# Kernel optimization log

Hardware: AMD Instinct MI355X
Metric: run time of the kernel (lower is better)

The kernel has to match this reference:

```python
import jax, jax.numpy as jnp
import numpy as np

N, E = 25000, 400000
F, D, H, C, L = 64, 128, 4, 128, 3  # in_feat, hidden, heads, per-head dim, layers
SCALE = 1.0 / np.sqrt(C)

_PNAMES = [f"{nm}{l}" for l in range(L) for nm in ("Wq", "bq", "Wk", "bk", "Wv", "bv", "Ws", "bs")]


def setup_inputs() -> dict:
    key = jax.random.key(0)
    ks = jax.random.split(key, 64)
    inp = {
        "x": jax.random.normal(ks[0], (N, F), jnp.float32),
        "edge_index": jax.random.randint(ks[1], (2, E), 0, N, jnp.int32),
    }
    i = 2
    for l in range(L):
        fin = F if l == 0 else D
        s = 1.0 / np.sqrt(fin)
        shapes = {"Wq": (fin, H * C), "bq": (H * C,), "Wk": (fin, H * C), "bk": (H * C,),
                  "Wv": (fin, H * C), "bv": (H * C,), "Ws": (fin, D), "bs": (D,)}
        for nm, shp in shapes.items():
            scale = s if nm.startswith("W") else 0.01
            inp[f"{nm}{l}"] = jax.random.normal(ks[i], shp, jnp.float32) * scale
            i += 1
    inp["Wfc"] = jax.random.normal(ks[i], (D, 1), jnp.float32) * (1.0 / np.sqrt(D))
    inp["bfc"] = jnp.zeros((1,), jnp.float32)
    return inp


def _conv(x, src, dst, Wq, bq, Wk, bk, Wv, bv, Ws, bs):
    """PyG TransformerConv, heads=H, concat=False (head-mean), root_weight=True."""
    n = x.shape[0]
    q = (x @ Wq + bq).reshape(n, H, C)
    k = (x @ Wk + bk).reshape(n, H, C)
    v = (x @ Wv + bv).reshape(n, H, C)
    # per-edge attention logits: query at dst, key at src  -> [E, H]
    alpha = jnp.einsum("ehc,ehc->eh", q[dst], k[src]) * SCALE
    # scatter-softmax over incoming edges of each destination node
    m = jax.ops.segment_max(alpha, dst, num_segments=n)        # [N, H]
    e = jnp.exp(alpha - m[dst])                                 # [E, H]
    denom = jax.ops.segment_sum(e, dst, num_segments=n)        # [N, H]
    a = e / (denom[dst] + 1e-16)                                # [E, H]
    out = jax.ops.segment_sum(a[:, :, None] * v[src], dst, num_segments=n)  # [N, H, C]
    return out.mean(axis=1) + x @ Ws + bs                       # concat=False -> mean heads; + skip


def reference(x, edge_index,
              Wq0, bq0, Wk0, bk0, Wv0, bv0, Ws0, bs0,
              Wq1, bq1, Wk1, bk1, Wv1, bv1, Ws1, bs1,
              Wq2, bq2, Wk2, bk2, Wv2, bv2, Ws2, bs2,
              Wfc, bfc):
    src, dst = edge_index[0], edge_index[1]
    h = jax.nn.relu(_conv(x, src, dst, Wq0, bq0, Wk0, bk0, Wv0, bv0, Ws0, bs0))
    h = jax.nn.relu(_conv(h, src, dst, Wq1, bq1, Wk1, bk1, Wv1, bv1, Ws1, bs1))
    h = jax.nn.relu(_conv(h, src, dst, Wq2, bq2, Wk2, bk2, Wv2, bv2, Ws2, bs2))
    g = h.mean(axis=0, keepdims=True)                           # [1, D]
    return jax.nn.sigmoid(g @ Wfc + bfc)                        # [1, 1]
```

## Files before the change

### kernel.cpp

```cpp
#include <hip/hip_runtime.h>
#include <hip/hip_bf16.h>
#include <math.h>

#define NNODES 25000
#define NEDGES 400000
#define FIN0 64
#define DHID 128
#define NHEAD 4
#define CDIM 128
#define HC (NHEAD * CDIM)
#define NOUT 1664
#define SCALE 0.088388347648318447f

typedef __attribute__((ext_vector_type(8))) short short8;
typedef __attribute__((ext_vector_type(4))) float floatx4;
typedef __attribute__((ext_vector_type(2))) float fx2;

__device__ __forceinline__ short f2bf(float v) {
    unsigned u = __float_as_uint(v);
    u = (u + 0x7fffu + ((u >> 16) & 1u)) >> 16;
    return (short)u;
}
__device__ __forceinline__ float bf2f(short s) {
    return __uint_as_float(((unsigned)(unsigned short)s) << 16);
}


__global__ void cvt_x_kernel(const float* __restrict__ x, short* __restrict__ xb, int total) {
    int i = blockIdx.x * blockDim.x + threadIdx.x;
    if (i < total) xb[i] = f2bf(x[i]);
}

__global__ __launch_bounds__(256) void cvt_w_kernel(
    const float* __restrict__ Wq, const float* __restrict__ Wk,
    const float* __restrict__ Wv, const float* __restrict__ Ws,
    const float* __restrict__ bq, const float* __restrict__ bk,
    const float* __restrict__ bv, const float* __restrict__ bs,
    short* __restrict__ WT, float* __restrict__ bc, int fin)
{
    __shared__ float tile[32][33];
    int c0 = blockIdx.x * 32;
    int k0 = blockIdx.y * 32;
    int tx = threadIdx.x & 31, ty = threadIdx.x >> 5;

    const float* W; int ldw, cb;
    if (c0 < 512)       { W = Wq; ldw = 512; cb = c0; }
    else if (c0 < 1024) { W = Wk; ldw = 512; cb = c0 - 512; }
    else if (c0 < 1536) { W = Wv; ldw = 512; cb = c0 - 1024; }
    else                { W = Ws; ldw = 128; cb = c0 - 1536; }

#pragma unroll
    for (int i = 0; i < 4; ++i) {
        int k = k0 + ty + i * 8;
        tile[ty + i * 8][tx] = W[(size_t)k * ldw + cb + tx];
    }
    __syncthreads();
#pragma unroll
    for (int i = 0; i < 4; ++i) {
        int c = c0 + ty + i * 8;
        WT[(size_t)c * fin + k0 + tx] = f2bf(tile[tx][ty + i * 8]);
    }

    if (blockIdx.y == 0 && ty == 0) {
        int c = c0 + tx;
        float b;
        if (c < 512)       b = bq[c];
        else if (c < 1024) b = bk[c - 512];
        else if (c < 1536) b = bv[c - 1024];
        else               b = bs[c - 1536];
        bc[c] = b;
    }
}


__global__ void count_kernel(const int* __restrict__ dst, int* __restrict__ deg, int e) {
    int i = blockIdx.x * blockDim.x + threadIdx.x;
    if (i < e) atomicAdd(&deg[dst[i]], 1);
}

__global__ void scan_kernel(const int* __restrict__ deg, int* __restrict__ offs,
                            int* __restrict__ cnt, int n, int total) {
    __shared__ int sums[256];
    int t = threadIdx.x;
    int chunk = (n + 255) / 256;
    int b = t * chunk;
    int e = min(b + chunk, n);
    int s = 0;
    for (int i = b; i < e; ++i) s += deg[i];
    sums[t] = s;
    __syncthreads();
    for (int o = 1; o < 256; o <<= 1) {
        int v = (t >= o) ? sums[t - o] : 0;
        __syncthreads();
        sums[t] += v;
        __syncthreads();
    }
    int run = sums[t] - s;
    for (int i = b; i < e; ++i) {
        offs[i] = run;
        run += deg[i];
        cnt[i] = 0;
    }
    if (t == 0) offs[n] = total;
}

__global__ void scatter_kernel(const int* __restrict__ src, const int* __restrict__ dst,
                               const int* __restrict__ offs, int* __restrict__ cnt,
                               int* __restrict__ csr, int e) {
    int i = blockIdx.x * blockDim.x + threadIdx.x;
    if (i < e) {
        int d = dst[i];
        int pos = offs[d] + atomicAdd(&cnt[d], 1);
        csr[pos] = src[i];
    }
}

template<int FIN>
__global__ __launch_bounds__(256) void gemm_qkvs_mfma(
    const short* __restrict__ Xb, int n,
    const short* __restrict__ WT, const float* __restrict__ bc,
    short* __restrict__ Qb, unsigned char* __restrict__ KV,
    short* __restrict__ Sb)
{
    constexpr int PITCH = FIN + 8;
    constexpr int CPR = FIN / 8;
    constexpr int NK = FIN / 32;
    __shared__ short Xs[64][PITCH];

    int t = threadIdx.x;
    int row0 = blockIdx.x * 64;
    int l = t & 63, w = t >> 6;
    int wcol = blockIdx.y * 256 + w * 64;
    bool active = (wcol < NOUT);
    int lr = l & 15, lk = (l >> 4) * 8;
    int cl = lr, rb = (l >> 4) * 4;

    short8 bfr[NK][4];
    if (active) {
#pragma unroll
        for (int ks = 0; ks < NK; ++ks)
#pragma unroll
            for (int ni = 0; ni < 4; ++ni)
                bfr[ks][ni] = *(const short8*)&WT[(size_t)(wcol + ni * 16 + lr) * FIN + ks * 32 + lk];
    }

    for (int i = t; i < 64 * CPR; i += 256) {
        int r = i / CPR, c = (i % CPR) * 8;
        int gr = row0 + r;
        uint4 v = make_uint4(0u, 0u, 0u, 0u);
        if (gr < n) v = *(const uint4*)&Xb[(size_t)gr * FIN + c];
        *(uint4*)&Xs[r][c] = v;
    }
    __syncthreads();
    if (!active) return;

    float bias[4];
#pragma unroll
    for (int ni = 0; ni < 4; ++ni) bias[ni] = bc[wcol + ni * 16 + cl];

    floatx4 acc[4][4] = {};
#pragma unroll
    for (int ks = 0; ks < NK; ++ks) {
        short8 a[4];
#pragma unroll
        for (int mi = 0; mi < 4; ++mi)
            a[mi] = *(const short8*)&Xs[mi * 16 + lr][ks * 32 + lk];
#pragma unroll
        for (int mi = 0; mi < 4; ++mi)
#pragma unroll
            for (int ni = 0; ni < 4; ++ni)
                acc[mi][ni] = __builtin_amdgcn_mfma_f32_16x16x32_bf16(
                    a[mi], bfr[ks][ni], acc[mi][ni], 0, 0, 0);
    }

    int kind = (wcol < 512) ? 0 : (wcol < 1024) ? 1 : (wcol < 1536) ? 2 : 3;
#pragma unroll
    for (int mi = 0; mi < 4; ++mi) {
#pragma unroll
        for (int ni = 0; ni < 4; ++ni) {
            int gc = wcol + ni * 16 + cl;
#pragma unroll
            for (int r = 0; r < 4; ++r) {
                int gr = row0 + mi * 16 + rb + r;
                if (gr >= n) continue;
                float v = acc[mi][ni][r] + bias[ni];
                if (kind == 0) {
                    Qb[(size_t)gr * 512 + gc] = f2bf(v);
                } else if (kind == 1) {
                    int c = gc - 512;
                    unsigned enc = (unsigned)__builtin_amdgcn_cvt_pk_fp8_f32(v, v, 0, false);
                    KV[(size_t)gr * 1024 + (c >> 3) * 16 + (c & 7)] = (unsigned char)enc;
                } else if (kind == 2) {
                    int c = gc - 1024;
                    unsigned enc = (unsigned)__builtin_amdgcn_cvt_pk_fp8_f32(v, v, 0, false);
                    KV[(size_t)gr * 1024 + (c >> 3) * 16 + 8 + (c & 7)] = (unsigned char)enc;
                } else {
                    Sb[(size_t)gr * 128 + (gc - 1536)] = f2bf(v);
                }
            }
        }
    }
}


__device__ __forceinline__ void unpack8(uint4 r, float* f) {
    f[0] = __uint_as_float(r.x << 16);
    f[1] = __uint_as_float(r.x & 0xffff0000u);
    f[2] = __uint_as_float(r.y << 16);
    f[3] = __uint_as_float(r.y & 0xffff0000u);
    f[4] = __uint_as_float(r.z << 16);
    f[5] = __uint_as_float(r.z & 0xffff0000u);
    f[6] = __uint_as_float(r.w << 16);
    f[7] = __uint_as_float(r.w & 0xffff0000u);
}

__device__ __forceinline__ void decf8(unsigned x, unsigned y, float* f) {
    fx2 a = __builtin_amdgcn_cvt_pk_f32_fp8(x, false);
    fx2 b = __builtin_amdgcn_cvt_pk_f32_fp8(x, true);
    fx2 c = __builtin_amdgcn_cvt_pk_f32_fp8(y, false);
    fx2 d = __builtin_amdgcn_cvt_pk_f32_fp8(y, true);
    f[0] = a[0]; f[1] = a[1]; f[2] = b[0]; f[3] = b[1];
    f[4] = c[0]; f[5] = c[1]; f[6] = d[0]; f[7] = d[1];
}

__device__ __forceinline__ float dotk(const float* q, uint4 kv) {
    float f[8];
    decf8(kv.x, kv.y, f);
    float p = 0.f;
#pragma unroll
    for (int j = 0; j < 8; ++j) p = fmaf(q[j], f[j], p);
    return p;
}

__device__ __forceinline__ void accv(float& d, float* acc, float p, uint4 kv) {
    float vf[8];
    decf8(kv.z, kv.w, vf);
    float w = __expf(p * SCALE);
    d += w;
#pragma unroll
    for (int j = 0; j < 8; ++j) acc[j] = fmaf(w, vf[j], acc[j]);
}

__device__ __forceinline__ float redu16(float p) {
#pragma unroll
    for (int o = 1; o < 16; o <<= 1) p += __shfl_xor(p, o);
    return p;
}

__global__ __launch_bounds__(256) void attn_kernel(
    const short* __restrict__ Qb, const unsigned char* __restrict__ KV,
    const int* __restrict__ offs, const int* __restrict__ csr,
    const short* __restrict__ Sb, short* __restrict__ Xo, int n)
{
    int node = (blockIdx.x * blockDim.x + threadIdx.x) >> 6;
    if (node >= n) return;
    int lane = threadIdx.x & 63;

    float qf[8];
    {
        uint4 qr = *(const uint4*)&Qb[(size_t)node * 512 + lane * 8];
        unpack8(qr, qf);
    }

    int beg = offs[node], end = offs[node + 1];
    float d = 0.f;
    float acc[8] = {};

    int e = beg;
    for (; e + 7 < end; e += 8) {
        uint4 kv[8];
#pragma unroll
        for (int j = 0; j < 8; ++j) {
            int s = csr[e + j];
            kv[j] = *(const uint4*)(KV + (size_t)s * 1024 + lane * 16);
        }
        float p[8];
#pragma unroll
        for (int j = 0; j < 8; ++j) p[j] = dotk(qf, kv[j]);
#pragma unroll
        for (int j = 0; j < 8; ++j) p[j] = redu16(p[j]);
#pragma unroll
        for (int j = 0; j < 8; ++j) accv(d, acc, p[j], kv[j]);
    }
    for (; e + 3 < end; e += 4) {
        uint4 kv[4];
#pragma unroll
        for (int j = 0; j < 4; ++j) {
            int s = csr[e + j];
            kv[j] = *(const uint4*)(KV + (size_t)s * 1024 + lane * 16);
        }
        float p[4];
#pragma unroll
        for (int j = 0; j < 4; ++j) p[j] = dotk(qf, kv[j]);
#pragma unroll
        for (int j = 0; j < 4; ++j) p[j] = redu16(p[j]);
#pragma unroll
        for (int j = 0; j < 4; ++j) accv(d, acc, p[j], kv[j]);
    }
    for (; e < end; ++e) {
        int s = csr[e];
        uint4 kv = *(const uint4*)(KV + (size_t)s * 1024 + lane * 16);
        float p = redu16(dotk(qf, kv));
        accv(d, acc, p, kv);
    }

    float inv = (d > 0.f) ? 1.f / d : 0.f;
#pragma unroll
    for (int j = 0; j < 8; ++j) acc[j] *= inv;

#pragma unroll
    for (int j = 0; j < 8; ++j) {
        acc[j] += __shfl_xor(acc[j], 16);
        acc[j] += __shfl_xor(acc[j], 32);
    }

    if (lane < 16) {
        int c0 = lane * 8;
        float sf[8];
        uint4 sr = *(const uint4*)&Sb[(size_t)node * 128 + c0];
        unpack8(sr, sf);
        short8 o;
#pragma unroll
        for (int j = 0; j < 8; ++j)
            o[j] = f2bf(fmaxf(acc[j] * 0.25f + sf[j], 0.f));
        *(short8*)&Xo[(size_t)node * 128 + c0] = o;
    }
}

__global__ void colsum_kernel(const short* __restrict__ X, float* __restrict__ g, int n) {
    int c = threadIdx.x;
    int rpb = (n + gridDim.x - 1) / gridDim.x;
    int r0 = blockIdx.x * rpb;
    int r1 = min(r0 + rpb, n);
    float acc = 0.f;
    for (int r = r0; r < r1; ++r) acc += bf2f(X[r * DHID + c]);
    atomicAdd(&g[c], acc);
}

__global__ void final_kernel(const float* __restrict__ g, const float* __restrict__ Wfc,
                             const float* __restrict__ bfc, float* __restrict__ out, float invn) {
    __shared__ float red[128];
    int t = threadIdx.x;
    red[t] = g[t] * invn * Wfc[t];
    __syncthreads();
    for (int o = 64; o > 0; o >>= 1) {
        if (t < o) red[t] += red[t + o];
        __syncthreads();
    }
    if (t == 0) {
        float z = red[0] + bfc[0];
        out[0] = 1.f / (1.f + expf(-z));
    }
}


extern "C" void kernel_launch(void* const* d_in, const int* in_sizes, int n_in,
                              void* d_out, int out_size, void* d_ws, size_t ws_size,
                              hipStream_t stream) {
    const int N = NNODES, E = NEDGES;
    const float* x = (const float*)d_in[0];
    const int* ei = (const int*)d_in[1];
    const int* src = ei;
    const int* dst = ei + E;
    const float* Wfc = (const float*)d_in[26];
    const float* bfc = (const float*)d_in[27];

    size_t off = 0;
    auto alloc = [&](size_t bytes) -> char* {
        char* p = (char*)d_ws + off;
        off += (bytes + 255) & ~(size_t)255;
        return p;
    };
    int* deg   = (int*)alloc((size_t)N * 4);
    int* cnt   = (int*)alloc((size_t)N * 4);
    int* offs  = (int*)alloc((size_t)(N + 1) * 4);
    int* csr   = (int*)alloc((size_t)E * 4);
    short* Qb  = (short*)alloc((size_t)N * HC * 2);
    unsigned char* KV = (unsigned char*)alloc((size_t)N * 1024);
    short* Sb  = (short*)alloc((size_t)N * DHID * 2);
    short* xb0 = (short*)alloc((size_t)(N + 64) * FIN0 * 2);
    short* xb1 = (short*)alloc((size_t)(N + 64) * DHID * 2);
    short* xb2 = (short*)alloc((size_t)(N + 64) * DHID * 2);
    short* WT  = (short*)alloc((size_t)NOUT * DHID * 2);
    float* bc  = (float*)alloc((size_t)NOUT * 4);
    float* g   = (float*)alloc(128 * 4);

    hipMemsetAsync(deg, 0, (size_t)N * 4, stream);
    hipMemsetAsync(g, 0, 128 * 4, stream);

    count_kernel<<<(E + 255) / 256, 256, 0, stream>>>(dst, deg, E);
    scan_kernel<<<1, 256, 0, stream>>>(deg, offs, cnt, N, E);
    scatter_kernel<<<(E + 255) / 256, 256, 0, stream>>>(src, dst, offs, cnt, csr, E);

    cvt_x_kernel<<<(N * FIN0 + 255) / 256, 256, 0, stream>>>(x, xb0, N * FIN0);

    int attn_blocks = (N + 3) / 4;

    const short* xin = xb0;
    short* xouts[3] = { xb1, xb2, xb1 };
    for (int l = 0; l < 3; ++l) {
        int fin = (l == 0) ? FIN0 : DHID;
        const float* Wq = (const float*)d_in[2 + l * 8 + 0];
        const float* bq = (const float*)d_in[2 + l * 8 + 1];
        const float* Wk = (const float*)d_in[2 + l * 8 + 2];
        const float* bk = (const float*)d_in[2 + l * 8 + 3];
        const float* Wv = (const float*)d_in[2 + l * 8 + 4];
        const float* bv = (const float*)d_in[2 + l * 8 + 5];
        const float* Wss= (const float*)d_in[2 + l * 8 + 6];
        const float* bs = (const float*)d_in[2 + l * 8 + 7];

        dim3 wgrid(NOUT / 32, fin / 32);
        cvt_w_kernel<<<wgrid, 256, 0, stream>>>(
            Wq, Wk, Wv, Wss, bq, bk, bv, bs, WT, bc, fin);

        dim3 ggrid((N + 63) / 64, 7);
        if (l == 0)
            gemm_qkvs_mfma<64><<<ggrid, 256, 0, stream>>>(xin, N, WT, bc, Qb, KV, Sb);
        else
            gemm_qkvs_mfma<128><<<ggrid, 256, 0, stream>>>(xin, N, WT, bc, Qb, KV, Sb);
        attn_kernel<<<attn_blocks, 256, 0, stream>>>(Qb, KV, offs, csr, Sb, xouts[l], N);
        xin = xouts[l];
    }

    colsum_kernel<<<256, 128, 0, stream>>>(xb1, g, N);
    final_kernel<<<1, 128, 0, stream>>>(g, Wfc, bfc, (float*)d_out, 1.0f / N);
}
```

Before: 596.8 us.

## Loop all output column tiles per block and split K/V into separate halves

```diff
diff --git a/kernel.cpp b/kernel.cpp
--- a/kernel.cpp
+++ b/kernel.cpp
@@ -130,19 +130,8 @@
     int t = threadIdx.x;
     int row0 = blockIdx.x * 64;
     int l = t & 63, w = t >> 6;
-    int wcol = blockIdx.y * 256 + w * 64;
-    bool active = (wcol < NOUT);
     int lr = l & 15, lk = (l >> 4) * 8;
     int cl = lr, rb = (l >> 4) * 4;
-
-    short8 bfr[NK][4];
-    if (active) {
-#pragma unroll
-        for (int ks = 0; ks < NK; ++ks)
-#pragma unroll
-            for (int ni = 0; ni < 4; ++ni)
-                bfr[ks][ni] = *(const short8*)&WT[(size_t)(wcol + ni * 16 + lr) * FIN + ks * 32 + lk];
-    }
 
     for (int i = t; i < 64 * CPR; i += 256) {
         int r = i / CPR, c = (i % CPR) * 8;
@@ -152,50 +141,56 @@
         *(uint4*)&Xs[r][c] = v;
     }
     __syncthreads();
-    if (!active) return;
-
-    float bias[4];
-#pragma unroll
-    for (int ni = 0; ni < 4; ++ni) bias[ni] = bc[wcol + ni * 16 + cl];
-
-    floatx4 acc[4][4] = {};
-#pragma unroll
-    for (int ks = 0; ks < NK; ++ks) {
-        short8 a[4];
-#pragma unroll
-        for (int mi = 0; mi < 4; ++mi)
-            a[mi] = *(const short8*)&Xs[mi * 16 + lr][ks * 32 + lk];
-#pragma unroll
-        for (int mi = 0; mi < 4; ++mi)
+
+    for (int y = 0; y < 7; ++y) {
+        int wcol = y * 256 + w * 64;
+        if (wcol >= NOUT) continue;
+
+        float bias[4];
+#pragma unroll
+        for (int ni = 0; ni < 4; ++ni) bias[ni] = bc[wcol + ni * 16 + cl];
+
+        floatx4 acc[4][4] = {};
+#pragma unroll
+        for (int ks = 0; ks < NK; ++ks) {
+            short8 b[4];
 #pragma unroll
             for (int ni = 0; ni < 4; ++ni)
-                acc[mi][ni] = __builtin_amdgcn_mfma_f32_16x16x32_bf16(
-                    a[mi], bfr[ks][ni], acc[mi][ni], 0, 0, 0);
-    }
-
-    int kind = (wcol < 512) ? 0 : (wcol < 1024) ? 1 : (wcol < 1536) ? 2 : 3;
-#pragma unroll
-    for (int mi = 0; mi < 4; ++mi) {
-#pragma unroll
-        for (int ni = 0; ni < 4; ++ni) {
-            int gc = wcol + ni * 16 + cl;
-#pragma unroll
-            for (int r = 0; r < 4; ++r) {
-                int gr = row0 + mi * 16 + rb + r;
-                if (gr >= n) continue;
-                float v = acc[mi][ni][r] + bias[ni];
-                if (kind == 0) {
-                    Qb[(size_t)gr * 512 + gc] = f2bf(v);
-                } else if (kind == 1) {
-                    int c = gc - 512;
-                    unsigned enc = (unsigned)__builtin_amdgcn_cvt_pk_fp8_f32(v, v, 0, false);
-                    KV[(size_t)gr * 1024 + (c >> 3) * 16 + (c & 7)] = (unsigned char)enc;
-                } else if (kind == 2) {
-                    int c = gc - 1024;
-                    unsigned enc = (unsigned)__builtin_amdgcn_cvt_pk_fp8_f32(v, v, 0, false);
-                    KV[(size_t)gr * 1024 + (c >> 3) * 16 + 8 + (c & 7)] = (unsigned char)enc;
-                } else {
-                    Sb[(size_t)gr * 128 + (gc - 1536)] = f2bf(v);
+                b[ni] = *(const short8*)&WT[(size_t)(wcol + ni * 16 + lr) * FIN + ks * 32 + lk];
+            short8 a[4];
+#pragma unroll
+            for (int mi = 0; mi < 4; ++mi)
+                a[mi] = *(const short8*)&Xs[mi * 16 + lr][ks * 32 + lk];
+#pragma unroll
+            for (int mi = 0; mi < 4; ++mi)
+#pragma unroll
+                for (int ni = 0; ni < 4; ++ni)
+                    acc[mi][ni] = __builtin_amdgcn_mfma_f32_16x16x32_bf16(
+                        a[mi], b[ni], acc[mi][ni], 0, 0, 0);
+        }
+
+        int kind = (wcol < 512) ? 0 : (wcol < 1024) ? 1 : (wcol < 1536) ? 2 : 3;
+#pragma unroll
+        for (int mi = 0; mi < 4; ++mi) {
+#pragma unroll
+            for (int ni = 0; ni < 4; ++ni) {
+                int gc = wcol + ni * 16 + cl;
+#pragma unroll
+                for (int r = 0; r < 4; ++r) {
+                    int gr = row0 + mi * 16 + rb + r;
+                    if (gr >= n) continue;
+                    float v = acc[mi][ni][r] + bias[ni];
+                    if (kind == 0) {
+                        Qb[(size_t)gr * 512 + gc] = f2bf(v);
+                    } else if (kind == 1) {
+                        unsigned enc = (unsigned)__builtin_amdgcn_cvt_pk_fp8_f32(v, v, 0, false);
+                        KV[(size_t)gr * 1024 + (gc - 512)] = (unsigned char)enc;
+                    } else if (kind == 2) {
+                        unsigned enc = (unsigned)__builtin_amdgcn_cvt_pk_fp8_f32(v, v, 0, false);
+                        KV[(size_t)gr * 1024 + 512 + (gc - 1024)] = (unsigned char)enc;
+                    } else {
+                        Sb[(size_t)gr * 128 + (gc - 1536)] = f2bf(v);
+                    }
                 }
             }
         }
@@ -223,18 +218,18 @@
     f[4] = c[0]; f[5] = c[1]; f[6] = d[0]; f[7] = d[1];
 }
 
-__device__ __forceinline__ float dotk(const float* q, uint4 kv) {
+__device__ __forceinline__ float dotk(const float* q, uint2 kr) {
     float f[8];
-    decf8(kv.x, kv.y, f);
+    decf8(kr.x, kr.y, f);
     float p = 0.f;
 #pragma unroll
     for (int j = 0; j < 8; ++j) p = fmaf(q[j], f[j], p);
     return p;
 }
 
-__device__ __forceinline__ void accv(float& d, float* acc, float p, uint4 kv) {
+__device__ __forceinline__ void accv(float& d, float* acc, float p, uint2 vr) {
     float vf[8];
-    decf8(kv.z, kv.w, vf);
+    decf8(vr.x, vr.y, vf);
     float w = __expf(p * SCALE);
     d += w;
 #pragma unroll
@@ -268,40 +263,46 @@
 
     int e = beg;
     for (; e + 7 < end; e += 8) {
-        uint4 kv[8];
+        uint2 kr[8], vr[8];
 #pragma unroll
         for (int j = 0; j < 8; ++j) {
             int s = csr[e + j];
-            kv[j] = *(const uint4*)(KV + (size_t)s * 1024 + lane * 16);
+            const unsigned char* b = KV + (size_t)s * 1024 + lane * 8;
+            kr[j] = *(const uint2*)b;
+            vr[j] = *(const uint2*)(b + 512);
         }
         float p[8];
 #pragma unroll
-        for (int j = 0; j < 8; ++j) p[j] = dotk(qf, kv[j]);
+        for (int j = 0; j < 8; ++j) p[j] = dotk(qf, kr[j]);
 #pragma unroll
         for (int j = 0; j < 8; ++j) p[j] = redu16(p[j]);
 #pragma unroll
-        for (int j = 0; j < 8; ++j) accv(d, acc, p[j], kv[j]);
+        for (int j = 0; j < 8; ++j) accv(d, acc, p[j], vr[j]);
     }
     for (; e + 3 < end; e += 4) {
-        uint4 kv[4];
+        uint2 kr[4], vr[4];
 #pragma unroll
         for (int j = 0; j < 4; ++j) {
             int s = csr[e + j];
-            kv[j] = *(const uint4*)(KV + (size_t)s * 1024 + lane * 16);
+            const unsigned char* b = KV + (size_t)s * 1024 + lane * 8;
+            kr[j] = *(const uint2*)b;
+            vr[j] = *(const uint2*)(b + 512);
         }
         float p[4];
 #pragma unroll
-        for (int j = 0; j < 4; ++j) p[j] = dotk(qf, kv[j]);
+        for (int j = 0; j < 4; ++j) p[j] = dotk(qf, kr[j]);
 #pragma unroll
         for (int j = 0; j < 4; ++j) p[j] = redu16(p[j]);
 #pragma unroll
-        for (int j = 0; j < 4; ++j) accv(d, acc, p[j], kv[j]);
+        for (int j = 0; j < 4; ++j) accv(d, acc, p[j], vr[j]);
     }
     for (; e < end; ++e) {
         int s = csr[e];
-        uint4 kv = *(const uint4*)(KV + (size_t)s * 1024 + lane * 16);
-        float p = redu16(dotk(qf, kv));
-        accv(d, acc, p, kv);
+        const unsigned char* b = KV + (size_t)s * 1024 + lane * 8;
+        uint2 kr = *(const uint2*)b;
+        uint2 vr = *(const uint2*)(b + 512);
+        float p = redu16(dotk(qf, kr));
+        accv(d, acc, p, vr);
     }
 
     float inv = (d > 0.f) ? 1.f / d : 0.f;
@@ -413,11 +414,11 @@
         cvt_w_kernel<<<wgrid, 256, 0, stream>>>(
             Wq, Wk, Wv, Wss, bq, bk, bv, bs, WT, bc, fin);
 
-        dim3 ggrid((N + 63) / 64, 7);
+        int gblocks = (N + 63) / 64;
         if (l == 0)
-            gemm_qkvs_mfma<64><<<ggrid, 256, 0, stream>>>(xin, N, WT, bc, Qb, KV, Sb);
+            gemm_qkvs_mfma<64><<<gblocks, 256, 0, stream>>>(xin, N, WT, bc, Qb, KV, Sb);
         else
-            gemm_qkvs_mfma<128><<<ggrid, 256, 0, stream>>>(xin, N, WT, bc, Qb, KV, Sb);
+            gemm_qkvs_mfma<128><<<gblocks, 256, 0, stream>>>(xin, N, WT, bc, Qb, KV, Sb);
         attn_kernel<<<attn_blocks, 256, 0, stream>>>(Qb, KV, offs, csr, Sb, xouts[l], N);
         xin = xouts[l];
     }
```

New measurement: 642.4 us. 7.6% more time.
